# Kernel optimization log

Measured on AMD Instinct MI355X. Metric: run time of the kernel, lower is better.

The kernel has to match this reference:

```python
import jax, jax.numpy as jnp
import numpy as np

N_ATOMS = 100000
ATOM_FDIM = 133
HIDDEN = 512
MAX_NEI = 6
N_MOLS = 4096
N_PAIRS = 8192


def setup_inputs() -> dict:
    key = jax.random.key(0)
    ks = jax.random.split(key, 12)
    s = 0.05  # weight init scale
    return {
        'f_atoms': jax.random.normal(ks[0], (N_ATOMS, ATOM_FDIM), jnp.float32),
        'a_neighbors': jax.random.randint(ks[1], (N_ATOMS, MAX_NEI), 0, N_ATOMS, dtype=jnp.int32),
        'mol_ids': jnp.sort(jax.random.randint(ks[2], (N_ATOMS,), 0, N_MOLS, dtype=jnp.int32)),
        'batch_edges': jax.random.randint(ks[3], (2, N_PAIRS), 0, N_MOLS, dtype=jnp.int32),
        'W_i': jax.random.normal(ks[4], (ATOM_FDIM, HIDDEN), jnp.float32) * s,
        'W_h': jax.random.normal(ks[5], (HIDDEN, HIDDEN), jnp.float32) * s,
        'W_o': jax.random.normal(ks[6], (ATOM_FDIM + HIDDEN, HIDDEN), jnp.float32) * s,
        'b_o': jnp.zeros((HIDDEN,), jnp.float32),
        'W_ffn_i': jax.random.normal(ks[7], (4 * HIDDEN, 2048), jnp.float32) * s,
        'b_ffn_i': jnp.zeros((2048,), jnp.float32),
        'W_ffn_1': jax.random.normal(ks[8], (2048, 1024), jnp.float32) * s,
        'b_ffn_1': jnp.zeros((1024,), jnp.float32),
        'W_ffn_2': jax.random.normal(ks[9], (1024, 1), jnp.float32) * s,
        'b_ffn_2': jnp.zeros((1,), jnp.float32),
    }


def reference(f_atoms, a_neighbors, mol_ids, batch_edges,
              W_i, W_h, W_o, b_o,
              W_ffn_i, b_ffn_i, W_ffn_1, b_ffn_1, W_ffn_2, b_ffn_2):
    # input = W_i(f_atoms); message = relu(input)
    inp = f_atoms @ W_i                      # [N, H]
    message = jax.nn.relu(inp)
    # neighbor gather + sum aggregation
    message = jnp.take(message, a_neighbors, axis=0).sum(axis=1)  # [N, H]
    # single message-passing layer (n_message_layer = 1), dropout=0 -> identity
    message = jax.nn.relu(inp + message @ W_h)
    # second gather + sum, then readout projection
    a_message = jnp.take(message, a_neighbors, axis=0).sum(axis=1)  # [N, H]
    a_input = jnp.concatenate([f_atoms, a_message], axis=1)         # [N, F+H]
    atom_hiddens = jax.nn.relu(a_input @ W_o + b_o)                 # [N, H]
    # segment-mean readout per molecule (empty segments -> zero vector)
    sums = jax.ops.segment_sum(atom_hiddens, mol_ids, num_segments=N_MOLS)
    counts = jax.ops.segment_sum(jnp.ones((atom_hiddens.shape[0], 1), atom_hiddens.dtype),
                                 mol_ids, num_segments=N_MOLS)
    mol_vecs = sums / jnp.maximum(counts, 1.0)                      # [M, H]
    # pairwise drug-drug features
    e1 = mol_vecs[batch_edges[0]]
    e2 = mol_vecs[batch_edges[1]]
    feature = jnp.concatenate([e1 + e2, e1 * e2, e1, e2], axis=1)   # [P, 4H]
    h = feature @ W_ffn_i + b_ffn_i
    h = jax.nn.relu(h) @ W_ffn_1 + b_ffn_1
    h = jax.nn.relu(h) @ W_ffn_2 + b_ffn_2
    return jax.nn.sigmoid(h).reshape(-1)                            # [P]
```

## Files before the change

kernel.cpp:

```cpp
#include <hip/hip_runtime.h>
#include <math.h>

#define N_ATOMS   100000
#define ATOM_FDIM 133
#define HIDDEN    512
#define MAX_NEI   6
#define N_MOLS    4096
#define N_PAIRS   8192

typedef __attribute__((ext_vector_type(8))) short short8;
typedef __attribute__((ext_vector_type(4))) float f32x4;
typedef __attribute__((ext_vector_type(2))) float f32x2;
typedef __attribute__((ext_vector_type(8))) int int8v;

static __device__ __forceinline__ float bf2f(unsigned short h) {
    return __uint_as_float(((unsigned int)h) << 16);
}
static __device__ __forceinline__ unsigned short f2bf(float f) {
    unsigned int u = __float_as_uint(f);
    u += 0x7FFFu + ((u >> 16) & 1u);
    return (unsigned short)(u >> 16);
}
static __device__ __forceinline__ unsigned int pk2bf(float a, float b) {
    unsigned int ua = __float_as_uint(a); ua += 0x7FFFu + ((ua >> 16) & 1u);
    unsigned int ub = __float_as_uint(b); ub += 0x7FFFu + ((ub >> 16) & 1u);
    return (ua >> 16) | (ub & 0xFFFF0000u);
}
static __device__ __forceinline__ unsigned int pk4f8(float a, float b, float c, float d) {
    unsigned int r = 0;
    r = __builtin_amdgcn_cvt_pk_fp8_f32(a, b, r, false);
    r = __builtin_amdgcn_cvt_pk_fp8_f32(c, d, r, true);
    return r;
}
static __device__ __forceinline__ void gl_lds16(const void* g, void* l) {
    __builtin_amdgcn_global_load_lds(
        (__attribute__((address_space(1))) void*)g,
        (__attribute__((address_space(3))) void*)l, 16, 0, 0);
}

__global__ __launch_bounds__(256)
void convert_f8(const float* __restrict__ in, unsigned char* __restrict__ out)
{
    int v = blockIdx.x * 256 + threadIdx.x;
    int row = v >> 4, sl = v & 15;
    int k0 = sl * 16;
    bool rok = row < N_ATOMS;
    const float* r = in + (size_t)row * ATOM_FDIM;
    float f[16];
#pragma unroll
    for (int e = 0; e < 16; ++e) {
        int kk = k0 + e;
        f[e] = (rok && kk < ATOM_FDIM) ? r[kk] : 0.f;
    }
    uint4 u;
    u.x = pk4f8(f[0], f[1], f[2], f[3]);
    u.y = pk4f8(f[4], f[5], f[6], f[7]);
    u.z = pk4f8(f[8], f[9], f[10], f[11]);
    u.w = pk4f8(f[12], f[13], f[14], f[15]);
    *(uint4*)(out + (size_t)row * 256 + k0) = u;
}

template<bool HAS_A0, bool RELU, bool HAS_BIAS, bool HAS_ADD, bool SWZ>
__global__ __launch_bounds__(256)
void gemm_f8(const unsigned char* __restrict__ A0, int lda0, int K0p,
             const unsigned char* __restrict__ A2, int lda2, int Kp,
             const unsigned char* __restrict__ Bt,
             const float* __restrict__ bias,
             const unsigned char* __restrict__ addm,
             unsigned char* __restrict__ C, int M, int N)
{
    __shared__ unsigned char lds[128 * 256];
    unsigned char* As = lds;
    unsigned char* Bs = lds + 128 * 128;
    unsigned short* Ct = (unsigned short*)lds;

    const int tid  = threadIdx.x;
    const int lane = tid & 63;
    const int wid  = tid >> 6;
    int bx, by;
    if (SWZ) {
        int L = blockIdx.y * gridDim.x + blockIdx.x;
        int xcd = L & 7, s = L >> 3;
        bx = s % gridDim.x;
        by = xcd + 8 * (s / gridDim.x);
    } else { bx = blockIdx.x; by = blockIdx.y; }
    const int row0 = by * 128;
    const int col0 = bx * 128;
    const int wm   = wid & 1, wn = wid >> 1;
    const int quad = lane >> 4, l15 = lane & 15;
    const int srow = lane >> 3, schunk = lane & 7;
    const int ssw  = (schunk ^ srow) * 16;

    f32x4 acc[4][4];
#pragma unroll
    for (int i = 0; i < 4; ++i)
#pragma unroll
        for (int j = 0; j < 4; ++j)
#pragma unroll
            for (int r = 0; r < 4; ++r) acc[i][j][r] = 0.f;

    for (int k0 = 0; k0 < Kp; k0 += 128) {
        __syncthreads();
        const unsigned char* Ak;
        int akof, alda;
        if (HAS_A0 && k0 < K0p) { Ak = A0; akof = k0; alda = lda0; }
        else { Ak = A2; akof = HAS_A0 ? (k0 - K0p) : k0; alda = lda2; }
#pragma unroll
        for (int i = 0; i < 4; ++i) {
            int mbase = wid * 32 + i * 8;
            int r = row0 + mbase + srow;
            gl_lds16(Ak + (size_t)r * alda + akof + ssw, &As[mbase * 128]);
        }
#pragma unroll
        for (int i = 0; i < 4; ++i) {
            int nbase = wid * 32 + i * 8;
            int rn = col0 + nbase + srow;
            gl_lds16(Bt + (size_t)rn * Kp + k0 + ssw, &Bs[nbase * 128]);
        }
        __syncthreads();
        const int s0 = ((2 * quad) ^ (l15 & 7)) * 16;
        const int s1 = ((2 * quad + 1) ^ (l15 & 7)) * 16;
        int8v a[4], b[4];
#pragma unroll
        for (int mt = 0; mt < 4; ++mt) {
            int r = wm * 64 + mt * 16 + l15;
            uint4 lo = *(const uint4*)&As[r * 128 + s0];
            uint4 hi = *(const uint4*)&As[r * 128 + s1];
            a[mt][0] = lo.x; a[mt][1] = lo.y; a[mt][2] = lo.z; a[mt][3] = lo.w;
            a[mt][4] = hi.x; a[mt][5] = hi.y; a[mt][6] = hi.z; a[mt][7] = hi.w;
        }
#pragma unroll
        for (int nt = 0; nt < 4; ++nt) {
            int r = wn * 64 + nt * 16 + l15;
            uint4 lo = *(const uint4*)&Bs[r * 128 + s0];
            uint4 hi = *(const uint4*)&Bs[r * 128 + s1];
            b[nt][0] = lo.x; b[nt][1] = lo.y; b[nt][2] = lo.z; b[nt][3] = lo.w;
            b[nt][4] = hi.x; b[nt][5] = hi.y; b[nt][6] = hi.z; b[nt][7] = hi.w;
        }
#pragma unroll
        for (int mt = 0; mt < 4; ++mt)
#pragma unroll
            for (int nt = 0; nt < 4; ++nt)
                acc[mt][nt] = __builtin_amdgcn_mfma_scale_f32_16x16x128_f8f6f4(
                    a[mt], b[nt], acc[mt][nt], 0, 0, 0, 127, 0, 127);
    }

    __syncthreads();
#pragma unroll
    for (int mt = 0; mt < 4; ++mt)
#pragma unroll
        for (int nt = 0; nt < 4; ++nt) {
            int cbase = wn * 64 + nt * 16 + l15;
            int rbase = wm * 64 + mt * 16 + quad * 4;
#pragma unroll
            for (int r = 0; r < 4; ++r)
                Ct[(rbase + r) * 128 + cbase] = f2bf(acc[mt][nt][r]);
        }
    __syncthreads();
#pragma unroll
    for (int i = 0; i < 8; ++i) {
        int c = tid + i * 256;
        int rr = c >> 4, cc = (c & 15) * 8;
        int m = row0 + rr, n = col0 + cc;
        short8 v = *(const short8*)&Ct[rr * 128 + cc];
        float f[8];
#pragma unroll
        for (int q = 0; q < 8; ++q) f[q] = bf2f((unsigned short)v[q]);
        if (HAS_BIAS) {
            float4 b0 = *(const float4*)(bias + n);
            float4 b1 = *(const float4*)(bias + n + 4);
            f[0] += b0.x; f[1] += b0.y; f[2] += b0.z; f[3] += b0.w;
            f[4] += b1.x; f[5] += b1.y; f[6] += b1.z; f[7] += b1.w;
        }
        if (m < M) {
            if (HAS_ADD) {
                uint2 ad = *(const uint2*)(addm + (size_t)m * N + n);
                f32x2 p;
                p = __builtin_amdgcn_cvt_pk_f32_fp8(ad.x, false); f[0] += p.x; f[1] += p.y;
                p = __builtin_amdgcn_cvt_pk_f32_fp8(ad.x, true);  f[2] += p.x; f[3] += p.y;
                p = __builtin_amdgcn_cvt_pk_f32_fp8(ad.y, false); f[4] += p.x; f[5] += p.y;
                p = __builtin_amdgcn_cvt_pk_f32_fp8(ad.y, true);  f[6] += p.x; f[7] += p.y;
            }
            if (RELU)
#pragma unroll
                for (int q = 0; q < 8; ++q) f[q] = fmaxf(f[q], 0.f);
            uint2 o;
            o.x = pk4f8(f[0], f[1], f[2], f[3]);
            o.y = pk4f8(f[4], f[5], f[6], f[7]);
            *(uint2*)(C + (size_t)m * N + n) = o;
        }
    }
}

template<bool RELU, bool HAS_BIAS, bool SWZ>
__global__ __launch_bounds__(256)
void gemm_bt(const unsigned short* __restrict__ A2, int lda2, int Kp,
             const unsigned short* __restrict__ Bt,
             const float* __restrict__ bias,
             unsigned short* __restrict__ C, int M, int N)
{
    __shared__ unsigned short lds[128 * 128];
    unsigned short* As = lds;
    unsigned short* Bs = lds + 128 * 64;
    unsigned short* Ct = lds;

    const int tid  = threadIdx.x;
    const int lane = tid & 63;
    const int wid  = tid >> 6;
    int bx, by;
    if (SWZ) {
        int L = blockIdx.y * gridDim.x + blockIdx.x;
        int xcd = L & 7, s = L >> 3;
        bx = s % gridDim.x;
        by = xcd + 8 * (s / gridDim.x);
    } else { bx = blockIdx.x; by = blockIdx.y; }
    const int row0 = by * 128;
    const int col0 = bx * 128;
    const int wm   = wid & 1, wn = wid >> 1;
    const int quad = lane >> 4, l15 = lane & 15;
    const int srow = lane >> 3;
    const int ssw  = ((lane & 7) ^ srow) * 8;

    f32x4 acc[4][4];
#pragma unroll
    for (int i = 0; i < 4; ++i)
#pragma unroll
        for (int j = 0; j < 4; ++j)
#pragma unroll
            for (int r = 0; r < 4; ++r) acc[i][j][r] = 0.f;

    for (int k0 = 0; k0 < Kp; k0 += 64) {
        __syncthreads();
#pragma unroll
        for (int i = 0; i < 4; ++i) {
            int mbase = wid * 32 + i * 8;
            int r = row0 + mbase + srow;
            gl_lds16(A2 + (size_t)r * lda2 + k0 + ssw, &As[mbase * 64]);
        }
#pragma unroll
        for (int i = 0; i < 4; ++i) {
            int nbase = wid * 32 + i * 8;
            int rn = col0 + nbase + srow;
            gl_lds16(Bt + (size_t)rn * Kp + k0 + ssw, &Bs[nbase * 64]);
        }
        __syncthreads();
#pragma unroll
        for (int ks = 0; ks < 2; ++ks) {
            int chunk = ks * 4 + quad;
            int slotA = (chunk ^ (l15 & 7)) * 8;
            short8 a[4], b[4];
#pragma unroll
            for (int mt = 0; mt < 4; ++mt)
                a[mt] = *(const short8*)&As[(wm * 64 + mt * 16 + l15) * 64 + slotA];
#pragma unroll
            for (int nt = 0; nt < 4; ++nt)
                b[nt] = *(const short8*)&Bs[(wn * 64 + nt * 16 + l15) * 64 + slotA];
#pragma unroll
            for (int mt = 0; mt < 4; ++mt)
#pragma unroll
                for (int nt = 0; nt < 4; ++nt)
                    acc[mt][nt] = __builtin_amdgcn_mfma_f32_16x16x32_bf16(
                        a[mt], b[nt], acc[mt][nt], 0, 0, 0);
        }
    }

    __syncthreads();
#pragma unroll
    for (int mt = 0; mt < 4; ++mt)
#pragma unroll
        for (int nt = 0; nt < 4; ++nt) {
            int cbase = wn * 64 + nt * 16 + l15;
            int rbase = wm * 64 + mt * 16 + quad * 4;
#pragma unroll
            for (int r = 0; r < 4; ++r)
                Ct[(rbase + r) * 128 + cbase] = f2bf(acc[mt][nt][r]);
        }
    __syncthreads();
#pragma unroll
    for (int i = 0; i < 8; ++i) {
        int c = tid + i * 256;
        int rr = c >> 4, cc = (c & 15) * 8;
        int m = row0 + rr, n = col0 + cc;
        short8 v = *(const short8*)&Ct[rr * 128 + cc];
        float f[8];
#pragma unroll
        for (int q = 0; q < 8; ++q) f[q] = bf2f((unsigned short)v[q]);
        if (HAS_BIAS) {
            float4 b0 = *(const float4*)(bias + n);
            float4 b1 = *(const float4*)(bias + n + 4);
            f[0] += b0.x; f[1] += b0.y; f[2] += b0.z; f[3] += b0.w;
            f[4] += b1.x; f[5] += b1.y; f[6] += b1.z; f[7] += b1.w;
        }
        if (RELU)
#pragma unroll
            for (int q = 0; q < 8; ++q) f[q] = fmaxf(f[q], 0.f);
        if (m < M) {
            uint4 o;
            o.x = pk2bf(f[0], f[1]); o.y = pk2bf(f[2], f[3]);
            o.z = pk2bf(f[4], f[5]); o.w = pk2bf(f[6], f[7]);
            *(uint4*)(C + (size_t)m * N + n) = o;
        }
    }
}

__global__ __launch_bounds__(256)
void transpose_bf16(const float* __restrict__ in, int K, int N,
                    unsigned short* __restrict__ out, int ldOut, int Kz, int koff)
{
    __shared__ float t[32][33];
    const int n0 = blockIdx.x * 32, k0 = blockIdx.y * 32;
    const int tx = threadIdx.x & 31, ty = threadIdx.x >> 5;
#pragma unroll
    for (int i = 0; i < 32; i += 8) {
        int k = k0 + ty + i, n = n0 + tx;
        t[ty + i][tx] = (k < K && n < N) ? in[(size_t)k * N + n] : 0.f;
    }
    __syncthreads();
#pragma unroll
    for (int i = 0; i < 32; i += 8) {
        int n = n0 + ty + i, k = k0 + tx;
        if (n < N && k < Kz)
            out[(size_t)n * ldOut + koff + k] = f2bf(t[tx][ty + i]);
    }
}

__global__ __launch_bounds__(256)
void transpose_f8(const float* __restrict__ in, int K, int N,
                  unsigned char* __restrict__ out, int ldOut, int Kz, int koff)
{
    __shared__ float t[32][33];
    const int n0 = blockIdx.x * 32, k0 = blockIdx.y * 32;
    const int tx = threadIdx.x & 31, ty = threadIdx.x >> 5;
#pragma unroll
    for (int i = 0; i < 32; i += 8) {
        int k = k0 + ty + i, n = n0 + tx;
        t[ty + i][tx] = (k < K && n < N) ? in[(size_t)k * N + n] : 0.f;
    }
    __syncthreads();
#pragma unroll
    for (int i = 0; i < 32; i += 8) {
        int n = n0 + ty + i, k = k0 + tx;
        if (n < N && k < Kz) {
            float v = t[tx][ty + i];
            out[(size_t)n * ldOut + koff + k] =
                (unsigned char)(__builtin_amdgcn_cvt_pk_fp8_f32(v, v, 0, false) & 0xFF);
        }
    }
}

__global__ __launch_bounds__(256)
void transpose_add_bf16(const float* __restrict__ inA, const float* __restrict__ inB,
                        int K, int N, unsigned short* __restrict__ out,
                        int ldOut, int koff)
{
    __shared__ float t[32][33];
    const int n0 = blockIdx.x * 32, k0 = blockIdx.y * 32;
    const int tx = threadIdx.x & 31, ty = threadIdx.x >> 5;
#pragma unroll
    for (int i = 0; i < 32; i += 8) {
        int k = k0 + ty + i, n = n0 + tx;
        float v = 0.f;
        if (k < K && n < N) {
            v = inA[(size_t)k * N + n];
            if (inB) v += inB[(size_t)k * N + n];
        }
        t[ty + i][tx] = v;
    }
    __syncthreads();
#pragma unroll
    for (int i = 0; i < 32; i += 8) {
        int n = n0 + ty + i, k = k0 + tx;
        if (n < N && k < K)
            out[(size_t)n * ldOut + koff + k] = f2bf(t[tx][ty + i]);
    }
}

template<bool RELU>
__global__ __launch_bounds__(256)
void gather_f8(const unsigned char* __restrict__ src,
               const int* __restrict__ nei, unsigned char* __restrict__ dst)
{
    const int atom = blockIdx.x * 8 + (threadIdx.x >> 5);
    const int l32  = threadIdx.x & 31;
    const int off  = l32 * 16;
    const int* np_ = nei + (size_t)atom * MAX_NEI;
    float s[16];
#pragma unroll
    for (int e = 0; e < 16; ++e) s[e] = 0.f;
#pragma unroll
    for (int j = 0; j < MAX_NEI; ++j) {
        uint4 u = *(const uint4*)(src + (size_t)np_[j] * HIDDEN + off);
        unsigned int w[4] = {u.x, u.y, u.z, u.w};
#pragma unroll
        for (int q = 0; q < 4; ++q) {
            f32x2 lo = __builtin_amdgcn_cvt_pk_f32_fp8(w[q], false);
            f32x2 hi = __builtin_amdgcn_cvt_pk_f32_fp8(w[q], true);
            float v0 = lo.x, v1 = lo.y, v2 = hi.x, v3 = hi.y;
            if (RELU) {
                v0 = fmaxf(v0, 0.f); v1 = fmaxf(v1, 0.f);
                v2 = fmaxf(v2, 0.f); v3 = fmaxf(v3, 0.f);
            }
            s[4 * q] += v0; s[4 * q + 1] += v1; s[4 * q + 2] += v2; s[4 * q + 3] += v3;
        }
    }
    uint4 o;
    o.x = pk4f8(s[0], s[1], s[2], s[3]);
    o.y = pk4f8(s[4], s[5], s[6], s[7]);
    o.z = pk4f8(s[8], s[9], s[10], s[11]);
    o.w = pk4f8(s[12], s[13], s[14], s[15]);
    *(uint4*)(dst + (size_t)atom * HIDDEN + off) = o;
}

__global__ __launch_bounds__(256)
void segmean_f8(const unsigned char* __restrict__ H,
                const int* __restrict__ mol_ids, float* __restrict__ molv)
{
    const int m = blockIdx.x;
    const int d = threadIdx.x * 2;
    int lo = 0, hi = N_ATOMS;
    while (lo < hi) { int mid = (lo + hi) >> 1; if (mol_ids[mid] < m) lo = mid + 1; else hi = mid; }
    const int start = lo;
    hi = N_ATOMS;
    while (lo < hi) { int mid = (lo + hi) >> 1; if (mol_ids[mid] < m + 1) lo = mid + 1; else hi = mid; }
    const int end = lo;
    float s0 = 0.f, s1 = 0.f;
    for (int a = start; a < end; ++a) {
        unsigned int raw = *(const unsigned short*)(H + (size_t)a * HIDDEN + d);
        f32x2 f = __builtin_amdgcn_cvt_pk_f32_fp8(raw, false);
        s0 += f.x; s1 += f.y;
    }
    int cnt = end - start;
    float inv = 1.0f / (float)(cnt > 0 ? cnt : 1);
    float2 o; o.x = s0 * inv; o.y = s1 * inv;
    *(float2*)(molv + (size_t)m * HIDDEN + d) = o;
}

__global__ __launch_bounds__(128)
void feature_kernel(const float* __restrict__ molv, const int* __restrict__ edges,
                    unsigned short* __restrict__ feat)
{
    const int p  = blockIdx.x;
    const int d4 = threadIdx.x * 4;
    const int i  = edges[p];
    const int j  = edges[N_PAIRS + p];
    float4 a = *(const float4*)(molv + (size_t)i * HIDDEN + d4);
    float4 b = *(const float4*)(molv + (size_t)j * HIDDEN + d4);
    unsigned short* o = feat + (size_t)p * 1536;
    uint2 w;
    w.x = pk2bf(a.x, a.y); w.y = pk2bf(a.z, a.w);
    *(uint2*)(o + d4) = w;
    w.x = pk2bf(b.x, b.y); w.y = pk2bf(b.z, b.w);
    *(uint2*)(o + HIDDEN + d4) = w;
    w.x = pk2bf(a.x * b.x, a.y * b.y); w.y = pk2bf(a.z * b.z, a.w * b.w);
    *(uint2*)(o + 2 * HIDDEN + d4) = w;
}

__global__ __launch_bounds__(256)
void final_kernel(const unsigned short* __restrict__ H, const float* __restrict__ w,
                  const float* __restrict__ b, float* __restrict__ out)
{
    const int p   = blockIdx.x;
    const int tid = threadIdx.x;
    const unsigned short* row = H + (size_t)p * 1024;
    float s = 0.f;
    for (int i = tid; i < 1024; i += 256) s += bf2f(row[i]) * w[i];
#pragma unroll
    for (int off = 32; off > 0; off >>= 1) s += __shfl_down(s, off, 64);
    __shared__ float red[4];
    if ((tid & 63) == 0) red[tid >> 6] = s;
    __syncthreads();
    if (tid == 0) {
        float t = red[0] + red[1] + red[2] + red[3] + b[0];
        out[p] = 1.0f / (1.0f + expf(-t));
    }
}

extern "C" void kernel_launch(void* const* d_in, const int* in_sizes, int n_in,
                              void* d_out, int out_size, void* d_ws, size_t ws_size,
                              hipStream_t stream)
{
    const float* f_atoms = (const float*)d_in[0];
    const int*   a_nei   = (const int*)d_in[1];
    const int*   mol_ids = (const int*)d_in[2];
    const int*   edges   = (const int*)d_in[3];
    const float* W_i     = (const float*)d_in[4];
    const float* W_h     = (const float*)d_in[5];
    const float* W_o     = (const float*)d_in[6];
    const float* b_o     = (const float*)d_in[7];
    const float* W_ffn_i = (const float*)d_in[8];
    const float* b_ffn_i = (const float*)d_in[9];
    const float* W_ffn_1 = (const float*)d_in[10];
    const float* b_ffn_1 = (const float*)d_in[11];
    const float* W_ffn_2 = (const float*)d_in[12];
    const float* b_ffn_2 = (const float*)d_in[13];
    float* out = (float*)d_out;

    char* ws = (char*)d_ws;
    unsigned char*  I     = (unsigned char*)ws;
    unsigned char*  Y     = (unsigned char*)(ws + 51200000);
    unsigned char*  Wt_i  = (unsigned char*)(ws + 102400000);
    unsigned char*  Wch   = (unsigned char*)(ws + 102531072);
    unsigned char*  Wco   = (unsigned char*)(ws + 102793216);
    float*          Mv    = (float*)(ws + 103186432);
    unsigned short* Wt_f0 = (unsigned short*)(ws + 111575040);
    unsigned short* Wt_f1 = (unsigned short*)(ws + 117866496);
    unsigned short* F     = (unsigned short*)(ws + 122060800);
    unsigned short* H1    = (unsigned short*)(ws + 147226624);
    unsigned short* H2    = (unsigned short*)(ws + 180781056);
    unsigned char*  Xf8   = (unsigned char*)(ws + 122060800);

    const float* W0 = W_ffn_i;
    const float* W1 = W_ffn_i + (size_t)512 * 2048;
    const float* W2 = W_ffn_i + (size_t)1024 * 2048;
    const float* W3 = W_ffn_i + (size_t)1536 * 2048;

    transpose_f8<<<dim3(16, 8),  256, 0, stream>>>(W_i, 133, 512, Wt_i, 256, 256, 0);
    transpose_f8<<<dim3(16, 16), 256, 0, stream>>>(W_h, 512, 512, Wch, 512, 512, 0);
    transpose_f8<<<dim3(16, 8),  256, 0, stream>>>(W_o, 133, 512, Wco, 768, 256, 0);
    transpose_f8<<<dim3(16, 16), 256, 0, stream>>>(W_o + (size_t)133 * 512,
                                                   512, 512, Wco, 768, 512, 256);
    transpose_add_bf16<<<dim3(64, 16), 256, 0, stream>>>(W0, W2, 512, 2048, Wt_f0, 1536, 0);
    transpose_add_bf16<<<dim3(64, 16), 256, 0, stream>>>(W0, W3, 512, 2048, Wt_f0, 1536, 512);
    transpose_add_bf16<<<dim3(64, 16), 256, 0, stream>>>(W1, nullptr, 512, 2048, Wt_f0, 1536, 1024);
    transpose_bf16<<<dim3(32, 64), 256, 0, stream>>>(W_ffn_1, 2048, 1024, Wt_f1, 2048, 2048, 0);

    convert_f8<<<100352 * 16 / 256, 256, 0, stream>>>(f_atoms, Xf8);

    gemm_f8<true, false, false, false, true><<<dim3(4, 784), 256, 0, stream>>>(
        Xf8, 256, 256, nullptr, 0, 256, Wt_i, nullptr, nullptr, I, N_ATOMS, HIDDEN);
    gather_f8<true><<<N_ATOMS / 8, 256, 0, stream>>>(I, a_nei, Y);
    gemm_f8<false, true, false, true, true><<<dim3(4, 784), 256, 0, stream>>>(
        nullptr, 0, 0, Y, 512, 512, Wch, nullptr, I, I, N_ATOMS, HIDDEN);
    gather_f8<false><<<N_ATOMS / 8, 256, 0, stream>>>(I, a_nei, Y);
    gemm_f8<true, true, true, false, true><<<dim3(4, 784), 256, 0, stream>>>(
        Xf8, 256, 256, Y, 512, 768, Wco, b_o, nullptr, I, N_ATOMS, HIDDEN);
    segmean_f8<<<N_MOLS, 256, 0, stream>>>(I, mol_ids, Mv);
    feature_kernel<<<N_PAIRS, 128, 0, stream>>>(Mv, edges, F);
    gemm_bt<true, true, true><<<dim3(16, 64), 256, 0, stream>>>(
        F, 1536, 1536, Wt_f0, b_ffn_i, H1, N_PAIRS, 2048);
    gemm_bt<true, true, true><<<dim3(8, 64), 256, 0, stream>>>(
        H1, 2048, 2048, Wt_f1, b_ffn_1, H2, N_PAIRS, 1024);
    final_kernel<<<N_PAIRS, 256, 0, stream>>>(H2, W_ffn_2, b_ffn_2, out);
    (void)in_sizes; (void)n_in; (void)out_size; (void)ws_size;
}
```

Measured before the change: 564.5 us.

## Replace FFN bf16 GEMM with double-buffered 256-row tile kernel

Replaces the 128x128 single-buffered FFN GEMM with a 512-thread kernel that uses 256xBN tiles and double-buffered LDS staging, so the next K tile loads while MFMAs run on the current one. It also raises MFMA priority around the compute block with s_setprio and drops the XCD swizzle and the M bounds check. Larger tiles improve operand reuse, but the grid shrinks to 256 blocks, which may underfill the CUs, and register and LDS pressure rise.

```diff
diff --git a/kernel.cpp b/kernel.cpp
--- a/kernel.cpp
+++ b/kernel.cpp
@@ -192,96 +192,122 @@
     }
 }
 
-template<bool RELU, bool HAS_BIAS, bool SWZ>
-__global__ __launch_bounds__(256)
-void gemm_bt(const unsigned short* __restrict__ A2, int lda2, int Kp,
-             const unsigned short* __restrict__ Bt,
-             const float* __restrict__ bias,
-             unsigned short* __restrict__ C, int M, int N)
-{
-    __shared__ unsigned short lds[128 * 128];
-    unsigned short* As = lds;
-    unsigned short* Bs = lds + 128 * 64;
-    unsigned short* Ct = lds;
+template<int NT, bool RELU, bool HAS_BIAS>
+__global__ __launch_bounds__(512, 2)
+void gemm_bt2(const unsigned short* __restrict__ A, int lda, int Kp,
+              const unsigned short* __restrict__ Bt,
+              const float* __restrict__ bias,
+              unsigned short* __restrict__ C, int M, int N)
+{
+    constexpr int BN = NT * 64;
+    constexpr int SMEM = 2 * 256 * 64 * 2 + 2 * BN * 64 * 2;
+    __shared__ unsigned char smem[SMEM];
+    unsigned short* As_ = (unsigned short*)smem;
+    unsigned short* Bs_ = (unsigned short*)(smem + 2 * 256 * 64 * 2);
+    unsigned short* Ct  = (unsigned short*)smem;
 
     const int tid  = threadIdx.x;
     const int lane = tid & 63;
     const int wid  = tid >> 6;
-    int bx, by;
-    if (SWZ) {
-        int L = blockIdx.y * gridDim.x + blockIdx.x;
-        int xcd = L & 7, s = L >> 3;
-        bx = s % gridDim.x;
-        by = xcd + 8 * (s / gridDim.x);
-    } else { bx = blockIdx.x; by = blockIdx.y; }
-    const int row0 = by * 128;
-    const int col0 = bx * 128;
-    const int wm   = wid & 1, wn = wid >> 1;
+    const int wr   = wid >> 2;
+    const int wc   = wid & 3;
     const int quad = lane >> 4, l15 = lane & 15;
-    const int srow = lane >> 3;
-    const int ssw  = ((lane & 7) ^ srow) * 8;
-
-    f32x4 acc[4][4];
-#pragma unroll
-    for (int i = 0; i < 4; ++i)
-#pragma unroll
-        for (int j = 0; j < 4; ++j)
+    const int srow = lane >> 3, schunk = lane & 7;
+    const int ssw  = (schunk ^ srow) * 8;
+
+    const int row0 = blockIdx.y * 256;
+    const int col0 = blockIdx.x * BN;
+
+    f32x4 acc[8][NT];
+#pragma unroll
+    for (int i = 0; i < 8; ++i)
+#pragma unroll
+        for (int j = 0; j < NT; ++j)
 #pragma unroll
             for (int r = 0; r < 4; ++r) acc[i][j][r] = 0.f;
 
-    for (int k0 = 0; k0 < Kp; k0 += 64) {
+#define STAGE_TILE(t, d)                                                     \
+    {                                                                        \
+        const int k0s = (t) * 64;                                            \
+        _Pragma("unroll")                                                    \
+        for (int i = 0; i < 4; ++i) {                                        \
+            int mbase = wid * 32 + i * 8;                                    \
+            int r = row0 + mbase + srow;                                     \
+            gl_lds16(A + (size_t)r * lda + k0s + ssw,                        \
+                     As_ + (d) * (256 * 64) + mbase * 64);                   \
+        }                                                                    \
+        _Pragma("unroll")                                                    \
+        for (int i = 0; i < NT; ++i) {                                       \
+            int nbase = wid * (NT * 8) + i * 8;                              \
+            int rn = col0 + nbase + srow;                                    \
+            gl_lds16(Bt + (size_t)rn * Kp + k0s + ssw,                       \
+                     Bs_ + (d) * (BN * 64) + nbase * 64);                    \
+        }                                                                    \
+    }
+
+    const int slot0 = ((quad) ^ (l15 & 7)) * 8;
+    const int slot1 = ((4 + quad) ^ (l15 & 7)) * 8;
+
+    const int ntiles = Kp >> 6;
+    STAGE_TILE(0, 0);
+    __syncthreads();
+
+    for (int t = 0; t < ntiles; ++t) {
+        const int d = t & 1;
+        if (t + 1 < ntiles) STAGE_TILE(t + 1, d ^ 1);
+
+        const int abase = d * (256 * 64);
+        const int bbase = d * (BN * 64);
+        short8 bf[NT][2];
+#pragma unroll
+        for (int nt2 = 0; nt2 < NT; ++nt2) {
+            int cn = wc * (NT * 16) + nt2 * 16 + l15;
+            bf[nt2][0] = *(const short8*)&Bs_[bbase + cn * 64 + slot0];
+            bf[nt2][1] = *(const short8*)&Bs_[bbase + cn * 64 + slot1];
+        }
+#pragma unroll
+        for (int q = 0; q < 4; ++q) {
+            short8 af[2][2];
+#pragma unroll
+            for (int j = 0; j < 2; ++j) {
+                int ar = wr * 128 + (q * 2 + j) * 16 + l15;
+                af[j][0] = *(const short8*)&As_[abase + ar * 64 + slot0];
+                af[j][1] = *(const short8*)&As_[abase + ar * 64 + slot1];
+            }
+            __builtin_amdgcn_s_setprio(1);
+#pragma unroll
+            for (int j = 0; j < 2; ++j)
+#pragma unroll
+                for (int nt2 = 0; nt2 < NT; ++nt2) {
+                    acc[q * 2 + j][nt2] = __builtin_amdgcn_mfma_f32_16x16x32_bf16(
+                        af[j][0], bf[nt2][0], acc[q * 2 + j][nt2], 0, 0, 0);
+                    acc[q * 2 + j][nt2] = __builtin_amdgcn_mfma_f32_16x16x32_bf16(
+                        af[j][1], bf[nt2][1], acc[q * 2 + j][nt2], 0, 0, 0);
+                }
+            __builtin_amdgcn_s_setprio(0);
+        }
         __syncthreads();
-#pragma unroll
-        for (int i = 0; i < 4; ++i) {
-            int mbase = wid * 32 + i * 8;
-            int r = row0 + mbase + srow;
-            gl_lds16(A2 + (size_t)r * lda2 + k0 + ssw, &As[mbase * 64]);
-        }
-#pragma unroll
-        for (int i = 0; i < 4; ++i) {
-            int nbase = wid * 32 + i * 8;
-            int rn = col0 + nbase + srow;
-            gl_lds16(Bt + (size_t)rn * Kp + k0 + ssw, &Bs[nbase * 64]);
-        }
-        __syncthreads();
-#pragma unroll
-        for (int ks = 0; ks < 2; ++ks) {
-            int chunk = ks * 4 + quad;
-            int slotA = (chunk ^ (l15 & 7)) * 8;
-            short8 a[4], b[4];
-#pragma unroll
-            for (int mt = 0; mt < 4; ++mt)
-                a[mt] = *(const short8*)&As[(wm * 64 + mt * 16 + l15) * 64 + slotA];
-#pragma unroll
-            for (int nt = 0; nt < 4; ++nt)
-                b[nt] = *(const short8*)&Bs[(wn * 64 + nt * 16 + l15) * 64 + slotA];
-#pragma unroll
-            for (int mt = 0; mt < 4; ++mt)
-#pragma unroll
-                for (int nt = 0; nt < 4; ++nt)
-                    acc[mt][nt] = __builtin_amdgcn_mfma_f32_16x16x32_bf16(
-                        a[mt], b[nt], acc[mt][nt], 0, 0, 0);
-        }
-    }
-
-    __syncthreads();
-#pragma unroll
-    for (int mt = 0; mt < 4; ++mt)
-#pragma unroll
-        for (int nt = 0; nt < 4; ++nt) {
-            int cbase = wn * 64 + nt * 16 + l15;
-            int rbase = wm * 64 + mt * 16 + quad * 4;
+    }
+#undef STAGE_TILE
+
+#pragma unroll
+    for (int mt = 0; mt < 8; ++mt)
+#pragma unroll
+        for (int nt2 = 0; nt2 < NT; ++nt2) {
+            int cbase = wc * (NT * 16) + nt2 * 16 + l15;
+            int rbase = wr * 128 + mt * 16 + quad * 4;
 #pragma unroll
             for (int r = 0; r < 4; ++r)
-                Ct[(rbase + r) * 128 + cbase] = f2bf(acc[mt][nt][r]);
-        }
-    __syncthreads();
-#pragma unroll
-    for (int i = 0; i < 8; ++i) {
-        int c = tid + i * 256;
-        int rr = c >> 4, cc = (c & 15) * 8;
+                Ct[(rbase + r) * BN + cbase] = f2bf(acc[mt][nt2][r]);
+        }
+    __syncthreads();
+    constexpr int NSTORE = 256 * BN / (512 * 8);
+#pragma unroll
+    for (int i = 0; i < NSTORE; ++i) {
+        int idx = (i * 512 + tid) * 8;
+        int rr = idx / BN, cc = idx % BN;
         int m = row0 + rr, n = col0 + cc;
-        short8 v = *(const short8*)&Ct[rr * 128 + cc];
+        short8 v = *(const short8*)&Ct[rr * BN + cc];
         float f[8];
 #pragma unroll
         for (int q = 0; q < 8; ++q) f[q] = bf2f((unsigned short)v[q]);
@@ -294,13 +320,12 @@
         if (RELU)
 #pragma unroll
             for (int q = 0; q < 8; ++q) f[q] = fmaxf(f[q], 0.f);
-        if (m < M) {
-            uint4 o;
-            o.x = pk2bf(f[0], f[1]); o.y = pk2bf(f[2], f[3]);
-            o.z = pk2bf(f[4], f[5]); o.w = pk2bf(f[6], f[7]);
-            *(uint4*)(C + (size_t)m * N + n) = o;
-        }
-    }
+        uint4 o;
+        o.x = pk2bf(f[0], f[1]); o.y = pk2bf(f[2], f[3]);
+        o.z = pk2bf(f[4], f[5]); o.w = pk2bf(f[6], f[7]);
+        *(uint4*)(C + (size_t)m * N + n) = o;
+    }
+    (void)M;
 }
 
 __global__ __launch_bounds__(256)
@@ -536,9 +561,9 @@
         Xf8, 256, 256, Y, 512, 768, Wco, b_o, nullptr, I, N_ATOMS, HIDDEN);
     segmean_f8<<<N_MOLS, 256, 0, stream>>>(I, mol_ids, Mv);
     feature_kernel<<<N_PAIRS, 128, 0, stream>>>(Mv, edges, F);
-    gemm_bt<true, true, true><<<dim3(16, 64), 256, 0, stream>>>(
+    gemm_bt2<4, true, true><<<dim3(8, 32), 512, 0, stream>>>(
         F, 1536, 1536, Wt_f0, b_ffn_i, H1, N_PAIRS, 2048);
-    gemm_bt<true, true, true><<<dim3(8, 64), 256, 0, stream>>>(
+    gemm_bt2<2, true, true><<<dim3(8, 32), 512, 0, stream>>>(
         H1, 2048, 2048, Wt_f1, b_ffn_1, H2, N_PAIRS, 1024);
     final_kernel<<<N_PAIRS, 256, 0, stream>>>(H2, W_ffn_2, b_ffn_2, out);
     (void)in_sizes; (void)n_in; (void)out_size; (void)ws_size;
```

Result: faster. 540.3 us (-4.3%).
